# Kernel optimization log

Measured on AMD Instinct MI355X. Metric: run time of the kernel, lower is better.

The kernel has to match this reference:

```python
import jax, jax.numpy as jnp
import numpy as np
import math

NUM_HEADS = 16
ROPE_BASE = 10000.0


def _rope_cos_sin(seq_len, head_dim, dtype):
    # Qwen2-style rotary embeddings. The torch source builds cos/sin of width
    # head_dim by concatenating freqs with itself, so the first and second
    # halves are identical; the half-width table below is the equivalent math.
    half = head_dim // 2
    inv_freq = 1.0 / (ROPE_BASE ** (jnp.arange(0, head_dim, 2, dtype=jnp.float32) / head_dim))
    t = jnp.arange(seq_len, dtype=jnp.float32)
    freqs = jnp.einsum('i,j->ij', t, inv_freq)  # [S, half]
    cos = jnp.cos(freqs).astype(dtype)[None, None]  # [1,1,S,half]
    sin = jnp.sin(freqs).astype(dtype)[None, None]
    return cos, sin


def _apply_rope(x, cos, sin):
    # x: [B, H, S, D]; split-half rotation (Qwen2 rotate-half convention)
    half = x.shape[-1] // 2
    x1, x2 = x[..., :half], x[..., half:]
    return jnp.concatenate([x1 * cos - x2 * sin, x2 * cos + x1 * sin], axis=-1)


def setup_inputs() -> dict:
    key = jax.random.key(0)
    ks = jax.random.split(key, 5)
    B, S, H = 2, 2048, 2048
    scale = 1.0 / math.sqrt(H)
    return {
        'hidden_states': jax.random.normal(ks[0], (B, S, H), dtype=jnp.float32),
        'Wq': jax.random.normal(ks[1], (H, H), dtype=jnp.float32) * scale,
        'Wk': jax.random.normal(ks[2], (H, H), dtype=jnp.float32) * scale,
        'Wv': jax.random.normal(ks[3], (H, H), dtype=jnp.float32) * scale,
        'Wo': jax.random.normal(ks[4], (H, H), dtype=jnp.float32) * scale,
    }


def reference(hidden_states, Wq, Wk, Wv, Wo):
    B, S, H = hidden_states.shape
    nh = NUM_HEADS
    hd = H // nh

    def proj(W):
        # nn.Linear: x @ W.T ; then [B,S,H] -> [B,nh,S,hd]
        y = jnp.einsum('bsh,oh->bso', hidden_states, W)
        return y.reshape(B, S, nh, hd).transpose(0, 2, 1, 3)

    q, k, v = proj(Wq), proj(Wk), proj(Wv)

    cos, sin = _rope_cos_sin(S, hd, hidden_states.dtype)
    q = _apply_rope(q, cos, sin)
    k = _apply_rope(k, cos, sin)

    scores = jnp.einsum('bhqd,bhkd->bhqk', q, k) / math.sqrt(hd)
    causal = jnp.triu(jnp.full((S, S), -jnp.inf, dtype=scores.dtype), k=1)
    scores = scores + causal[None, None]
    probs = jax.nn.softmax(scores, axis=-1)

    ctx = jnp.einsum('bhqk,bhkd->bhqd', probs, v)  # [B,nh,S,hd]
    ctx = ctx.transpose(0, 2, 1, 3).reshape(B, S, H)
    out = jnp.einsum('bsh,oh->bso', ctx, Wo)
    return out
```

## Files before the change

kernel.cpp:

```cpp
#include <hip/hip_runtime.h>

#define S_LEN 2048
#define HID   2048
#define NHEAD 16
#define HD    128
#define BSZ   2
#define BS_TOT (BSZ * S_LEN)
#define QKS   4096

typedef __bf16 bf16x8 __attribute__((ext_vector_type(8)));
typedef unsigned short u16x8 __attribute__((ext_vector_type(8)));
typedef unsigned short u16x4 __attribute__((ext_vector_type(4)));
typedef float f32x4 __attribute__((ext_vector_type(4)));

static __device__ __forceinline__ bf16x8 as_bf(u16x8 v) { return __builtin_bit_cast(bf16x8, v); }

static __device__ __forceinline__ unsigned short f2bf(float f) {
  __bf16 h = (__bf16)f;
  return __builtin_bit_cast(unsigned short, h);
}
static __device__ __forceinline__ float bf2f(unsigned short b) {
  unsigned int u = ((unsigned int)b) << 16;
  return __builtin_bit_cast(float, u);
}

static __device__ __forceinline__ void gload_lds16(const unsigned short* g, unsigned short* l) {
  __builtin_amdgcn_global_load_lds((const __attribute__((address_space(1))) unsigned int*)g,
                                   (__attribute__((address_space(3))) unsigned int*)l, 16, 0, 0);
}

__global__ __launch_bounds__(256) void cvt_all(const float* __restrict__ hs,
                                               const float* __restrict__ Wq,
                                               const float* __restrict__ Wk,
                                               const float* __restrict__ Wv,
                                               const float* __restrict__ Wo,
                                               unsigned short* __restrict__ hsb,
                                               unsigned short* __restrict__ wall,
                                               float* __restrict__ ct, float* __restrict__ st) {
  int b = (int)blockIdx.x, tid = (int)threadIdx.x;
  if (b < 8192) {
    int i = b * 256 + tid;
    float4 v = ((const float4*)hs)[i];
    ushort4 o; o.x = f2bf(v.x); o.y = f2bf(v.y); o.z = f2bf(v.z); o.w = f2bf(v.w);
    ((ushort4*)hsb)[i] = o;
  } else if (b < 24576) {
    int t = b - 8192;
    int wsel = t >> 12;
    const float* in = (wsel == 0) ? Wq : (wsel == 1) ? Wk : (wsel == 2) ? Wv : Wo;
    int i = (t & 4095) * 256 + tid;
    float4 v = ((const float4*)in)[i];
    ushort4 o; o.x = f2bf(v.x); o.y = f2bf(v.y); o.z = f2bf(v.z); o.w = f2bf(v.w);
    ((ushort4*)(wall + (size_t)wsel * HID * HID))[i] = o;
  } else {
    int id = (b - 24576) * 256 + tid;
    int tt = id >> 6, d = id & 63;
    float inv = powf(10000.0f, -(float)d * (1.0f / 64.0f));
    float f = (float)tt * inv;
    float sv, cv;
    sincosf(f, &sv, &cv);
    ct[id] = cv; st[id] = sv;
  }
}

__global__ __launch_bounds__(256) void rope_apply(unsigned short* __restrict__ qk,
                                                  const float* __restrict__ ct,
                                                  const float* __restrict__ st) {
  int id = blockIdx.x * 256 + threadIdx.x;
  int d = id & 63;
  int h = (id >> 6) & (NHEAD - 1);
  int m = id >> 10;
  int s = m & (S_LEN - 1);
  float c = ct[s * 64 + d], sn = st[s * 64 + d];
  size_t base = (size_t)m * QKS + h * HD + d;
  float q1 = bf2f(qk[base]), q2 = bf2f(qk[base + 64]);
  qk[base]      = f2bf(q1 * c - q2 * sn);
  qk[base + 64] = f2bf(q2 * c + q1 * sn);
  float k1 = bf2f(qk[base + 2048]), k2 = bf2f(qk[base + 2048 + 64]);
  qk[base + 2048]      = f2bf(k1 * c - k2 * sn);
  qk[base + 2048 + 64] = f2bf(k2 * c + k1 * sn);
}

template <typename OutT>
__global__ __launch_bounds__(256) void gemm_bt(const unsigned short* __restrict__ A,
                                               const unsigned short* __restrict__ Bw,
                                               OutT* __restrict__ C, int M, int N, int K) {
  __shared__ __align__(16) unsigned short As[4][128 * 32];
  __shared__ __align__(16) unsigned short Bs[4][128 * 32];
  int x = (int)blockIdx.x;
  int chunk = (int)gridDim.x >> 3;
  int x2 = (x & 7) * chunk + (x >> 3);
  const int nbn = N >> 7;
  int bm = x2 / nbn, bn = x2 % nbn;
  int tid = (int)threadIdx.x;
  int l = tid & 63, lr = l & 15, lg = l >> 4;
  int w = tid >> 6, wm = w >> 1, wn = w & 1;

  int w32 = 32 * w;
  int srow = w32 + (l >> 2);
  int ssw = ((l >> 2) ^ (l >> 4)) & 3;
  const unsigned short* gA = A + (size_t)(bm * 128 + srow) * K + (((l & 3) ^ ssw) << 3);
  const unsigned short* gB = Bw + (size_t)(bn * 128 + srow) * K + (((l & 3) ^ ssw) << 3);

  int rsw = (lr ^ (lr >> 2)) & 3;
  int aoff[4], boff[4];
#pragma unroll
  for (int i = 0; i < 4; ++i) {
    aoff[i] = (wm * 64 + i * 16 + lr) * 32 + ((lg ^ rsw) << 3);
    boff[i] = (wn * 64 + i * 16 + lr) * 32 + ((lg ^ rsw) << 3);
  }

  f32x4 zero = {0.f, 0.f, 0.f, 0.f};
  f32x4 acc[4][4];
#pragma unroll
  for (int mi = 0; mi < 4; ++mi)
#pragma unroll
    for (int ni = 0; ni < 4; ++ni) acc[mi][ni] = zero;

  int nk = K >> 5;

#define STAGE(buf, kt)                                                        \
  do {                                                                        \
    const unsigned short* pa_ = gA + (size_t)(kt) * 32;                       \
    const unsigned short* pb_ = gB + (size_t)(kt) * 32;                       \
    gload_lds16(pa_, &As[buf][w32 * 32]);                                     \
    gload_lds16(pa_ + (size_t)16 * K, &As[buf][(w32 + 16) * 32]);             \
    gload_lds16(pb_, &Bs[buf][w32 * 32]);                                     \
    gload_lds16(pb_ + (size_t)16 * K, &Bs[buf][(w32 + 16) * 32]);             \
  } while (0)

#define COMPUTE(buf)                                                          \
  do {                                                                        \
    u16x8 af[4], bfr[4];                                                      \
    _Pragma("unroll") for (int i = 0; i < 4; ++i) {                           \
      af[i] = *(const u16x8*)&As[buf][aoff[i]];                               \
      bfr[i] = *(const u16x8*)&Bs[buf][boff[i]];                              \
    }                                                                         \
    _Pragma("unroll") for (int mi = 0; mi < 4; ++mi)                          \
        _Pragma("unroll") for (int ni = 0; ni < 4; ++ni)                      \
            acc[mi][ni] = __builtin_amdgcn_mfma_f32_16x16x32_bf16(            \
                as_bf(af[mi]), as_bf(bfr[ni]), acc[mi][ni], 0, 0, 0);         \
  } while (0)

  STAGE(0, 0);
  STAGE(1, 1);
  STAGE(2, 2);
  asm volatile("s_waitcnt vmcnt(8)" ::: "memory");
  __builtin_amdgcn_s_barrier();
#pragma unroll 4
  for (int kt = 0; kt < nk; ++kt) {
    COMPUTE(kt & 3);
    asm volatile("s_waitcnt vmcnt(4) lgkmcnt(0)" ::: "memory");
    __builtin_amdgcn_s_barrier();
    STAGE((kt + 3) & 3, (kt + 3) & (nk - 1));
  }
#undef STAGE
#undef COMPUTE

#pragma unroll
  for (int mi = 0; mi < 4; ++mi) {
#pragma unroll
    for (int ni = 0; ni < 4; ++ni) {
      int col = bn * 128 + wn * 64 + ni * 16 + lr;
#pragma unroll
      for (int j = 0; j < 4; ++j) {
        int rowm = bm * 128 + wm * 64 + mi * 16 + 4 * lg + j;
        float v = acc[mi][ni][j];
        if constexpr (sizeof(OutT) == 2) C[(size_t)rowm * N + col] = f2bf(v);
        else                             C[(size_t)rowm * N + col] = v;
      }
    }
  }
  (void)M;
}

__global__ __launch_bounds__(256, 2) void attn_fwd(const unsigned short* __restrict__ qk,
                                                   const unsigned short* __restrict__ vt,
                                                   unsigned short* __restrict__ ctx) {
  __shared__ __align__(16) unsigned short Ks[2][64 * 128];
  __shared__ __align__(16) unsigned short Vs[2][128 * 64];
  __shared__ __align__(16) unsigned short Ps[4 * 32 * 64];

  int x = (int)blockIdx.x;
  int bh, qt;
  if (x < 256) { bh = x & 31;         qt = 15 - (x >> 5); }
  else         { bh = (x - 256) & 31; qt = (x - 256) >> 5; }
  int b = bh >> 4, h = bh & 15;
  int q0 = qt * 128;
  int nt = 2 * qt + 2;

  int tid = (int)threadIdx.x;
  int w = tid >> 6, l = tid & 63, lr = l & 15, lg = l >> 4;
  const float CEXP = 0.12751744f;
  const float THRRAW = 90.509668f;
  const int bS = b * S_LEN, h128 = h * HD;
  const int qw = q0 + w * 32;
  const unsigned short* qg = qk;
  const unsigned short* kg = qk + 2048;

  u16x8 qfr[2][4];
#pragma unroll
  for (int qf = 0; qf < 2; ++qf) {
    const unsigned short* qb = qg + (size_t)(bS + qw + qf * 16 + lr) * QKS + h128;
#pragma unroll
    for (int kk = 0; kk < 4; ++kk) qfr[qf][kk] = *(const u16x8*)(qb + kk * 32 + lg * 8);
  }

  const unsigned short* kbg[4];
  const unsigned short* vbg[4];
#pragma unroll
  for (int i = 0; i < 4; ++i) {
    int rr = 16 * w + 4 * i + (l >> 4);
    int colK = ((l & 15) ^ (rr & 15)) * 8;
    kbg[i] = kg + (size_t)(bS + rr) * QKS + h128 + colK;
    int vd = 32 * w + 8 * i + (l >> 3);
    int colV = ((l & 7) ^ (vd & 7)) * 8;
    vbg[i] = vt + (size_t)(h128 + vd) * BS_TOT + bS + colV;
  }

#define ASTAGE(buf, t)                                                        \
  do {                                                                        \
    size_t koff_ = (size_t)(t) * 64 * QKS;                                    \
    int voff_ = (t) * 64;                                                     \
    _Pragma("unroll") for (int i_ = 0; i_ < 4; ++i_) {                        \
      gload_lds16(kbg[i_] + koff_, &Ks[buf][(16 * w + 4 * i_) * 128]);        \
      gload_lds16(vbg[i_] + voff_, &Vs[buf][(32 * w + 8 * i_) * 64]);         \
    }                                                                         \
  } while (0)

  f32x4 zero = {0.f, 0.f, 0.f, 0.f};
  f32x4 oacc[2][8];
#pragma unroll
  for (int qf = 0; qf < 2; ++qf)
#pragma unroll
    for (int nj = 0; nj < 8; ++nj) oacc[qf][nj] = zero;
  float mrow[2] = {-1e30f, -1e30f}, lsum[2] = {0.f, 0.f};

  int cur = 0;
  ASTAGE(0, 0);
  __syncthreads();

  for (int t = 0; t < nt; ++t) {
    int k0 = t * 64;
    if (t + 1 < nt) ASTAGE(cur ^ 1, t + 1);

    if (k0 <= qw + 31) {
      const unsigned short* KsB = &Ks[cur][0];
      const unsigned short* VsB = &Vs[cur][0];
      f32x4 sac[2][4];
#pragma unroll
      for (int qf = 0; qf < 2; ++qf)
#pragma unroll
        for (int ni = 0; ni < 4; ++ni) sac[qf][ni] = zero;
      __builtin_amdgcn_s_setprio(1);
#pragma unroll
      for (int kk = 0; kk < 4; ++kk) {
#pragma unroll
        for (int ni = 0; ni < 4; ++ni) {
          u16x8 kf = *(const u16x8*)&KsB[(ni * 16 + lr) * 128 + (((kk * 4 + lg) ^ lr) * 8)];
          sac[0][ni] = __builtin_amdgcn_mfma_f32_16x16x32_bf16(as_bf(kf), as_bf(qfr[0][kk]), sac[0][ni], 0, 0, 0);
          sac[1][ni] = __builtin_amdgcn_mfma_f32_16x16x32_bf16(as_bf(kf), as_bf(qfr[1][kk]), sac[1][ni], 0, 0, 0);
        }
      }
      __builtin_amdgcn_s_setprio(0);
      bool needmask = (k0 + 63 > qw);

#pragma unroll
      for (int qf = 0; qf < 2; ++qf) {
        float s[4][4];
#pragma unroll
        for (int ni = 0; ni < 4; ++ni)
#pragma unroll
          for (int j = 0; j < 4; ++j) s[ni][j] = sac[qf][ni][j];
        if (needmask) {
          int qgl = qw + qf * 16 + lr;
#pragma unroll
          for (int ni = 0; ni < 4; ++ni)
#pragma unroll
            for (int j = 0; j < 4; ++j)
              if (k0 + ni * 16 + 4 * lg + j > qgl) s[ni][j] = -1e30f;
        }
        float mx = s[0][0];
#pragma unroll
        for (int ni = 0; ni < 4; ++ni)
#pragma unroll
          for (int j = 0; j < 4; ++j) mx = fmaxf(mx, s[ni][j]);
        mx = fmaxf(mx, __shfl_xor(mx, 16));
        mx = fmaxf(mx, __shfl_xor(mx, 32));
        if (!__all(mx - mrow[qf] <= THRRAW)) {
          float mn = fmaxf(mrow[qf], mx);
          float al = exp2f((mrow[qf] - mn) * CEXP);
          mrow[qf] = mn;
          lsum[qf] *= al;
          float a0 = __shfl(al, 4 * lg + 0, 16);
          float a1 = __shfl(al, 4 * lg + 1, 16);
          float a2 = __shfl(al, 4 * lg + 2, 16);
          float a3 = __shfl(al, 4 * lg + 3, 16);
#pragma unroll
          for (int nj = 0; nj < 8; ++nj) {
            oacc[qf][nj][0] *= a0; oacc[qf][nj][1] *= a1;
            oacc[qf][nj][2] *= a2; oacc[qf][nj][3] *= a3;
          }
        }
        float m = mrow[qf];
        float rs = 0.f;
#pragma unroll
        for (int ni = 0; ni < 4; ++ni)
#pragma unroll
          for (int j = 0; j < 4; ++j) {
            float p = exp2f((s[ni][j] - m) * CEXP);
            s[ni][j] = p; rs += p;
          }
        lsum[qf] += rs;
        unsigned short* pw = &Ps[w * 2048];
#pragma unroll
        for (int ni = 0; ni < 4; ++ni) {
          u16x4 pv = {f2bf(s[ni][0]), f2bf(s[ni][1]), f2bf(s[ni][2]), f2bf(s[ni][3])};
          *(u16x4*)&pw[(qf * 16 + lr) * 64 + (((2 * ni + (lg >> 1)) ^ (lr & 7)) * 8) + (lg & 1) * 4] = pv;
        }
      }

      const unsigned short* pw = &Ps[w * 2048];
      __builtin_amdgcn_s_setprio(1);
#pragma unroll
      for (int kk2 = 0; kk2 < 2; ++kk2) {
        u16x8 pa0 = *(const u16x8*)&pw[(0 * 16 + lr) * 64 + (((kk2 * 4 + lg) ^ (lr & 7)) * 8)];
        u16x8 pa1 = *(const u16x8*)&pw[(1 * 16 + lr) * 64 + (((kk2 * 4 + lg) ^ (lr & 7)) * 8)];
#pragma unroll
        for (int nj = 0; nj < 8; ++nj) {
          u16x8 vf = *(const u16x8*)&VsB[(nj * 16 + lr) * 64 + (((kk2 * 4 + lg) ^ (lr & 7)) * 8)];
          oacc[0][nj] = __builtin_amdgcn_mfma_f32_16x16x32_bf16(as_bf(pa0), as_bf(vf), oacc[0][nj], 0, 0, 0);
          oacc[1][nj] = __builtin_amdgcn_mfma_f32_16x16x32_bf16(as_bf(pa1), as_bf(vf), oacc[1][nj], 0, 0, 0);
        }
      }
      __builtin_amdgcn_s_setprio(0);
    }

    __syncthreads();
    cur ^= 1;
  }
#undef ASTAGE

#pragma unroll
  for (int qf = 0; qf < 2; ++qf) {
    float ls = lsum[qf];
    ls += __shfl_xor(ls, 16);
    ls += __shfl_xor(ls, 32);
    float rl = 1.0f / ls;
    float r0 = __shfl(rl, 4 * lg + 0, 16);
    float r1 = __shfl(rl, 4 * lg + 1, 16);
    float r2 = __shfl(rl, 4 * lg + 2, 16);
    float r3 = __shfl(rl, 4 * lg + 3, 16);
    size_t obase = (size_t)(bS + qw + qf * 16 + 4 * lg) * HID + h128;
#pragma unroll
    for (int nj = 0; nj < 8; ++nj) {
      ctx[obase + 0 * HID + nj * 16 + lr] = f2bf(oacc[qf][nj][0] * r0);
      ctx[obase + 1 * HID + nj * 16 + lr] = f2bf(oacc[qf][nj][1] * r1);
      ctx[obase + 2 * HID + nj * 16 + lr] = f2bf(oacc[qf][nj][2] * r2);
      ctx[obase + 3 * HID + nj * 16 + lr] = f2bf(oacc[qf][nj][3] * r3);
    }
  }
}

extern "C" void kernel_launch(void* const* d_in, const int* in_sizes, int n_in,
                              void* d_out, int out_size, void* d_ws, size_t ws_size,
                              hipStream_t stream) {
  const float* hs = (const float*)d_in[0];
  const float* Wq = (const float*)d_in[1];
  const float* Wk = (const float*)d_in[2];
  const float* Wv = (const float*)d_in[3];
  const float* Wo = (const float*)d_in[4];

  char* ws = (char*)d_ws;
  unsigned short* hsb  = (unsigned short*)(ws);
  unsigned short* wall = (unsigned short*)(ws + 16777216);
  unsigned short* qkb  = (unsigned short*)(ws + 50331648);
  unsigned short* vtb  = (unsigned short*)(ws + 83886080);
  float* ctab = (float*)(ws + 100663296);
  float* stab = (float*)(ws + 101187584);
  unsigned short* ctxb = hsb;

  cvt_all<<<25088, 256, 0, stream>>>(hs, Wq, Wk, Wv, Wo, hsb, wall, ctab, stab);

  gemm_bt<unsigned short><<<1024, 256, 0, stream>>>(hsb, wall, qkb, BS_TOT, 2 * HID, HID);
  gemm_bt<unsigned short><<<512, 256, 0, stream>>>(wall + 2 * (size_t)HID * HID, hsb, vtb, HID, BS_TOT, HID);

  rope_apply<<<16384, 256, 0, stream>>>(qkb, ctab, stab);

  attn_fwd<<<512, 256, 0, stream>>>(qkb, vtb, ctxb);

  gemm_bt<float><<<512, 256, 0, stream>>>(ctxb, wall + 3 * (size_t)HID * HID, (float*)d_out, BS_TOT, HID, HID);

  (void)in_sizes; (void)n_in; (void)out_size; (void)ws_size;
}
```

Baseline: 296.3 us.

## Widen GEMM tile to 128x256 with triple buffering and vectorize RoPE

The GEMM tile grows from 128x128 to 128x256. Each warp now owns a full 128-row by 64-column slice, using 8x4 MFMA accumulators and a 3-stage LDS pipeline, with a manually unrolled loop and launch bounds set for 2 blocks per SM. This raises arithmetic intensity per LDS load but halves the block counts (256/512 blocks), so GPU fill and register pressure are at risk. Separately, the RoPE kernel now processes 4 elements per thread with vector loads and stores.

```diff
diff --git a/kernel.cpp b/kernel.cpp
--- a/kernel.cpp
+++ b/kernel.cpp
@@ -66,53 +66,63 @@
                                                   const float* __restrict__ ct,
                                                   const float* __restrict__ st) {
   int id = blockIdx.x * 256 + threadIdx.x;
-  int d = id & 63;
-  int h = (id >> 6) & (NHEAD - 1);
-  int m = id >> 10;
+  int d4 = (id & 15) * 4;
+  int h = (id >> 4) & (NHEAD - 1);
+  int m = id >> 8;
   int s = m & (S_LEN - 1);
-  float c = ct[s * 64 + d], sn = st[s * 64 + d];
-  size_t base = (size_t)m * QKS + h * HD + d;
-  float q1 = bf2f(qk[base]), q2 = bf2f(qk[base + 64]);
-  qk[base]      = f2bf(q1 * c - q2 * sn);
-  qk[base + 64] = f2bf(q2 * c + q1 * sn);
-  float k1 = bf2f(qk[base + 2048]), k2 = bf2f(qk[base + 2048 + 64]);
-  qk[base + 2048]      = f2bf(k1 * c - k2 * sn);
-  qk[base + 2048 + 64] = f2bf(k2 * c + k1 * sn);
+  float4 c  = *(const float4*)(ct + s * 64 + d4);
+  float4 sn = *(const float4*)(st + s * 64 + d4);
+  size_t base = (size_t)m * QKS + h * HD + d4;
+  u16x4 q1 = *(u16x4*)(qk + base), q2 = *(u16x4*)(qk + base + 64);
+  u16x4 k1 = *(u16x4*)(qk + base + 2048), k2 = *(u16x4*)(qk + base + 2048 + 64);
+  u16x4 o1, o2, p1, p2;
+  float cc[4] = {c.x, c.y, c.z, c.w}, ss[4] = {sn.x, sn.y, sn.z, sn.w};
+#pragma unroll
+  for (int j = 0; j < 4; ++j) {
+    float a = bf2f(q1[j]), bq = bf2f(q2[j]);
+    o1[j] = f2bf(a * cc[j] - bq * ss[j]);
+    o2[j] = f2bf(bq * cc[j] + a * ss[j]);
+    float ak = bf2f(k1[j]), bk = bf2f(k2[j]);
+    p1[j] = f2bf(ak * cc[j] - bk * ss[j]);
+    p2[j] = f2bf(bk * cc[j] + ak * ss[j]);
+  }
+  *(u16x4*)(qk + base) = o1;
+  *(u16x4*)(qk + base + 64) = o2;
+  *(u16x4*)(qk + base + 2048) = p1;
+  *(u16x4*)(qk + base + 2048 + 64) = p2;
 }
 
 template <typename OutT>
-__global__ __launch_bounds__(256) void gemm_bt(const unsigned short* __restrict__ A,
-                                               const unsigned short* __restrict__ Bw,
-                                               OutT* __restrict__ C, int M, int N, int K) {
-  __shared__ __align__(16) unsigned short As[4][128 * 32];
-  __shared__ __align__(16) unsigned short Bs[4][128 * 32];
+__global__ __launch_bounds__(256, 2) void gemm_bt(const unsigned short* __restrict__ A,
+                                                  const unsigned short* __restrict__ Bw,
+                                                  OutT* __restrict__ C, int M, int N, int K) {
+  __shared__ __align__(16) unsigned short As[3][128 * 32];
+  __shared__ __align__(16) unsigned short Bs[3][256 * 32];
   int x = (int)blockIdx.x;
   int chunk = (int)gridDim.x >> 3;
   int x2 = (x & 7) * chunk + (x >> 3);
-  const int nbn = N >> 7;
+  const int nbn = N >> 8;
   int bm = x2 / nbn, bn = x2 % nbn;
   int tid = (int)threadIdx.x;
   int l = tid & 63, lr = l & 15, lg = l >> 4;
-  int w = tid >> 6, wm = w >> 1, wn = w & 1;
-
-  int w32 = 32 * w;
-  int srow = w32 + (l >> 2);
+  int w = tid >> 6;
+  int w32 = 32 * w, w64 = 64 * w;
+
   int ssw = ((l >> 2) ^ (l >> 4)) & 3;
-  const unsigned short* gA = A + (size_t)(bm * 128 + srow) * K + (((l & 3) ^ ssw) << 3);
-  const unsigned short* gB = Bw + (size_t)(bn * 128 + srow) * K + (((l & 3) ^ ssw) << 3);
+  const unsigned short* gA = A + (size_t)(bm * 128 + w32 + (l >> 2)) * K + (((l & 3) ^ ssw) << 3);
+  const unsigned short* gB = Bw + (size_t)(bn * 256 + w64 + (l >> 2)) * K + (((l & 3) ^ ssw) << 3);
 
   int rsw = (lr ^ (lr >> 2)) & 3;
-  int aoff[4], boff[4];
-#pragma unroll
-  for (int i = 0; i < 4; ++i) {
-    aoff[i] = (wm * 64 + i * 16 + lr) * 32 + ((lg ^ rsw) << 3);
-    boff[i] = (wn * 64 + i * 16 + lr) * 32 + ((lg ^ rsw) << 3);
-  }
+  int aoff[8], boff[4];
+#pragma unroll
+  for (int i = 0; i < 8; ++i) aoff[i] = (i * 16 + lr) * 32 + ((lg ^ rsw) << 3);
+#pragma unroll
+  for (int i = 0; i < 4; ++i) boff[i] = (w64 + i * 16 + lr) * 32 + ((lg ^ rsw) << 3);
 
   f32x4 zero = {0.f, 0.f, 0.f, 0.f};
-  f32x4 acc[4][4];
-#pragma unroll
-  for (int mi = 0; mi < 4; ++mi)
+  f32x4 acc[8][4];
+#pragma unroll
+  for (int mi = 0; mi < 8; ++mi)
 #pragma unroll
     for (int ni = 0; ni < 4; ++ni) acc[mi][ni] = zero;
 
@@ -124,46 +134,56 @@
     const unsigned short* pb_ = gB + (size_t)(kt) * 32;                       \
     gload_lds16(pa_, &As[buf][w32 * 32]);                                     \
     gload_lds16(pa_ + (size_t)16 * K, &As[buf][(w32 + 16) * 32]);             \
-    gload_lds16(pb_, &Bs[buf][w32 * 32]);                                     \
-    gload_lds16(pb_ + (size_t)16 * K, &Bs[buf][(w32 + 16) * 32]);             \
+    gload_lds16(pb_, &Bs[buf][w64 * 32]);                                     \
+    gload_lds16(pb_ + (size_t)16 * K, &Bs[buf][(w64 + 16) * 32]);             \
+    gload_lds16(pb_ + (size_t)32 * K, &Bs[buf][(w64 + 32) * 32]);             \
+    gload_lds16(pb_ + (size_t)48 * K, &Bs[buf][(w64 + 48) * 32]);             \
   } while (0)
 
 #define COMPUTE(buf)                                                          \
   do {                                                                        \
-    u16x8 af[4], bfr[4];                                                      \
-    _Pragma("unroll") for (int i = 0; i < 4; ++i) {                           \
-      af[i] = *(const u16x8*)&As[buf][aoff[i]];                               \
-      bfr[i] = *(const u16x8*)&Bs[buf][boff[i]];                              \
-    }                                                                         \
-    _Pragma("unroll") for (int mi = 0; mi < 4; ++mi)                          \
+    u16x8 af[8], bfr[4];                                                      \
+    _Pragma("unroll") for (int i = 0; i < 8; ++i)                             \
+        af[i] = *(const u16x8*)&As[buf][aoff[i]];                             \
+    _Pragma("unroll") for (int i = 0; i < 4; ++i)                             \
+        bfr[i] = *(const u16x8*)&Bs[buf][boff[i]];                            \
+    _Pragma("unroll") for (int mi = 0; mi < 8; ++mi)                          \
         _Pragma("unroll") for (int ni = 0; ni < 4; ++ni)                      \
             acc[mi][ni] = __builtin_amdgcn_mfma_f32_16x16x32_bf16(            \
                 as_bf(af[mi]), as_bf(bfr[ni]), acc[mi][ni], 0, 0, 0);         \
   } while (0)
 
+#define BODY(b)                                                               \
+  do {                                                                        \
+    COMPUTE(b);                                                               \
+    asm volatile("s_waitcnt vmcnt(6) lgkmcnt(0)" ::: "memory");               \
+    __builtin_amdgcn_s_barrier();                                             \
+    STAGE(b, (kt + 3) & (nk - 1));                                            \
+    ++kt;                                                                     \
+  } while (0)
+
   STAGE(0, 0);
   STAGE(1, 1);
   STAGE(2, 2);
-  asm volatile("s_waitcnt vmcnt(8)" ::: "memory");
+  asm volatile("s_waitcnt vmcnt(12)" ::: "memory");
   __builtin_amdgcn_s_barrier();
-#pragma unroll 4
-  for (int kt = 0; kt < nk; ++kt) {
-    COMPUTE(kt & 3);
-    asm volatile("s_waitcnt vmcnt(4) lgkmcnt(0)" ::: "memory");
-    __builtin_amdgcn_s_barrier();
-    STAGE((kt + 3) & 3, (kt + 3) & (nk - 1));
-  }
+
+  int kt = 0;
+  while (kt + 3 <= nk) { BODY(0); BODY(1); BODY(2); }
+  if (kt < nk) BODY(0);
+  if (kt < nk) BODY(1);
+#undef BODY
 #undef STAGE
 #undef COMPUTE
 
 #pragma unroll
-  for (int mi = 0; mi < 4; ++mi) {
+  for (int mi = 0; mi < 8; ++mi) {
 #pragma unroll
     for (int ni = 0; ni < 4; ++ni) {
-      int col = bn * 128 + wn * 64 + ni * 16 + lr;
+      int col = bn * 256 + w64 + ni * 16 + lr;
 #pragma unroll
       for (int j = 0; j < 4; ++j) {
-        int rowm = bm * 128 + wm * 64 + mi * 16 + 4 * lg + j;
+        int rowm = bm * 128 + mi * 16 + 4 * lg + j;
         float v = acc[mi][ni][j];
         if constexpr (sizeof(OutT) == 2) C[(size_t)rowm * N + col] = f2bf(v);
         else                             C[(size_t)rowm * N + col] = v;
@@ -381,14 +401,14 @@
 
   cvt_all<<<25088, 256, 0, stream>>>(hs, Wq, Wk, Wv, Wo, hsb, wall, ctab, stab);
 
-  gemm_bt<unsigned short><<<1024, 256, 0, stream>>>(hsb, wall, qkb, BS_TOT, 2 * HID, HID);
-  gemm_bt<unsigned short><<<512, 256, 0, stream>>>(wall + 2 * (size_t)HID * HID, hsb, vtb, HID, BS_TOT, HID);
-
-  rope_apply<<<16384, 256, 0, stream>>>(qkb, ctab, stab);
+  gemm_bt<unsigned short><<<512, 256, 0, stream>>>(hsb, wall, qkb, BS_TOT, 2 * HID, HID);
+  gemm_bt<unsigned short><<<256, 256, 0, stream>>>(wall + 2 * (size_t)HID * HID, hsb, vtb, HID, BS_TOT, HID);
+
+  rope_apply<<<4096, 256, 0, stream>>>(qkb, ctab, stab);
 
   attn_fwd<<<512, 256, 0, stream>>>(qkb, vtb, ctxb);
 
-  gemm_bt<float><<<512, 256, 0, stream>>>(ctxb, wall + 3 * (size_t)HID * HID, (float*)d_out, BS_TOT, HID, HID);
+  gemm_bt<float><<<256, 256, 0, stream>>>(ctxb, wall + 3 * (size_t)HID * HID, (float*)d_out, BS_TOT, HID, HID);
 
   (void)in_sizes; (void)n_in; (void)out_size; (void)ws_size;
 }
```

New measurement: 316.5 us. 1.07x slower.

## Add 256x256-tile GEMM for QK projection and vectorize RoPE kernel

Applied to the files above, without the earlier changes.

Adds a new 512-thread GEMM kernel with 256x256 output tiles, BK=64 double-buffered LDS staging with XOR swizzle and setprio around MFMA bursts. It is used for the fused Q/K projection to raise arithmetic intensity per block. The RoPE kernel also now processes four elements per thread with vector loads and stores, cutting its launch to a quarter of the threads. The large tile produces only 256 blocks on a 256-CU device, which gives a single wave with no tail but leaves little latency hiding per CU.

```diff
diff --git a/kernel.cpp b/kernel.cpp
--- a/kernel.cpp
+++ b/kernel.cpp
@@ -66,22 +66,131 @@
                                                   const float* __restrict__ ct,
                                                   const float* __restrict__ st) {
   int id = blockIdx.x * 256 + threadIdx.x;
-  int d = id & 63;
-  int h = (id >> 6) & (NHEAD - 1);
-  int m = id >> 10;
+  int d4 = (id & 15) * 4;
+  int h = (id >> 4) & (NHEAD - 1);
+  int m = id >> 8;
   int s = m & (S_LEN - 1);
-  float c = ct[s * 64 + d], sn = st[s * 64 + d];
-  size_t base = (size_t)m * QKS + h * HD + d;
-  float q1 = bf2f(qk[base]), q2 = bf2f(qk[base + 64]);
-  qk[base]      = f2bf(q1 * c - q2 * sn);
-  qk[base + 64] = f2bf(q2 * c + q1 * sn);
-  float k1 = bf2f(qk[base + 2048]), k2 = bf2f(qk[base + 2048 + 64]);
-  qk[base + 2048]      = f2bf(k1 * c - k2 * sn);
-  qk[base + 2048 + 64] = f2bf(k2 * c + k1 * sn);
+  float4 c  = *(const float4*)(ct + s * 64 + d4);
+  float4 sn = *(const float4*)(st + s * 64 + d4);
+  size_t base = (size_t)m * QKS + h * HD + d4;
+  u16x4 q1 = *(u16x4*)(qk + base), q2 = *(u16x4*)(qk + base + 64);
+  u16x4 k1 = *(u16x4*)(qk + base + 2048), k2 = *(u16x4*)(qk + base + 2048 + 64);
+  u16x4 o1, o2, p1, p2;
+  float cc[4] = {c.x, c.y, c.z, c.w}, ss[4] = {sn.x, sn.y, sn.z, sn.w};
+#pragma unroll
+  for (int j = 0; j < 4; ++j) {
+    float a = bf2f(q1[j]), bq = bf2f(q2[j]);
+    o1[j] = f2bf(a * cc[j] - bq * ss[j]);
+    o2[j] = f2bf(bq * cc[j] + a * ss[j]);
+    float ak = bf2f(k1[j]), bk = bf2f(k2[j]);
+    p1[j] = f2bf(ak * cc[j] - bk * ss[j]);
+    p2[j] = f2bf(bk * cc[j] + ak * ss[j]);
+  }
+  *(u16x4*)(qk + base) = o1;
+  *(u16x4*)(qk + base + 64) = o2;
+  *(u16x4*)(qk + base + 2048) = p1;
+  *(u16x4*)(qk + base + 2048 + 64) = p2;
 }
 
 template <typename OutT>
-__global__ __launch_bounds__(256) void gemm_bt(const unsigned short* __restrict__ A,
+__global__ __launch_bounds__(512, 1) void gemm256(const unsigned short* __restrict__ A,
+                                                  const unsigned short* __restrict__ Bw,
+                                                  OutT* __restrict__ C, int M, int N, int K) {
+  __shared__ __align__(16) unsigned short As[2][256 * 64];
+  __shared__ __align__(16) unsigned short Bs[2][256 * 64];
+  int x = (int)blockIdx.x;
+  int chunk = (int)gridDim.x >> 3;
+  int x2 = (x & 7) * chunk + (x >> 3);
+  const int nbn = N >> 8;
+  int bm = x2 / nbn, bn = x2 % nbn;
+  int tid = (int)threadIdx.x;
+  int l = tid & 63, lr = l & 15, lg = l >> 4;
+  int w = tid >> 6;
+  int wm = w >> 2, wn = w & 3;
+
+  int srow = 32 * w + (l >> 3);
+  int sslot = (l & 7) ^ ((l >> 3) & 7);
+  const unsigned short* gA = A + (size_t)(bm * 256 + srow) * K + sslot * 8;
+  const unsigned short* gB = Bw + (size_t)(bn * 256 + srow) * K + sslot * 8;
+
+  int rs7 = lr & 7;
+
+  f32x4 zero = {0.f, 0.f, 0.f, 0.f};
+  f32x4 acc[8][4];
+#pragma unroll
+  for (int mi = 0; mi < 8; ++mi)
+#pragma unroll
+    for (int ni = 0; ni < 4; ++ni) acc[mi][ni] = zero;
+
+  int nk = K >> 6;
+
+#define STAGE256(buf, kt)                                                       \
+  do {                                                                          \
+    size_t ko_ = (size_t)(kt) * 64;                                             \
+    _Pragma("unroll") for (int i_ = 0; i_ < 4; ++i_) {                          \
+      gload_lds16(gA + (size_t)(8 * i_) * K + ko_, &As[buf][(32 * w + 8 * i_) * 64]); \
+      gload_lds16(gB + (size_t)(8 * i_) * K + ko_, &Bs[buf][(32 * w + 8 * i_) * 64]); \
+    }                                                                           \
+  } while (0)
+
+  STAGE256(0, 0);
+  __syncthreads();
+
+  for (int kt = 0; kt < nk; ++kt) {
+    if (kt + 1 < nk) STAGE256((kt + 1) & 1, kt + 1);
+    const unsigned short* Ab = &As[kt & 1][0];
+    const unsigned short* Bb = &Bs[kt & 1][0];
+
+    u16x8 bfr[4][2];
+#pragma unroll
+    for (int ni = 0; ni < 4; ++ni)
+#pragma unroll
+      for (int ks = 0; ks < 2; ++ks)
+        bfr[ni][ks] = *(const u16x8*)&Bb[(wn * 64 + ni * 16 + lr) * 64 + (((ks * 4 + lg) ^ rs7) * 8)];
+
+#pragma unroll
+    for (int mq = 0; mq < 4; ++mq) {
+      u16x8 af[2][2];
+#pragma unroll
+      for (int m2 = 0; m2 < 2; ++m2)
+#pragma unroll
+        for (int ks = 0; ks < 2; ++ks)
+          af[m2][ks] = *(const u16x8*)&Ab[(wm * 128 + (2 * mq + m2) * 16 + lr) * 64 + (((ks * 4 + lg) ^ rs7) * 8)];
+      __builtin_amdgcn_s_setprio(1);
+#pragma unroll
+      for (int m2 = 0; m2 < 2; ++m2)
+#pragma unroll
+        for (int ni = 0; ni < 4; ++ni)
+#pragma unroll
+          for (int ks = 0; ks < 2; ++ks)
+            acc[2 * mq + m2][ni] = __builtin_amdgcn_mfma_f32_16x16x32_bf16(
+                as_bf(af[m2][ks]), as_bf(bfr[ni][ks]), acc[2 * mq + m2][ni], 0, 0, 0);
+      __builtin_amdgcn_s_setprio(0);
+      __builtin_amdgcn_s_barrier();
+    }
+    __syncthreads();
+  }
+#undef STAGE256
+
+#pragma unroll
+  for (int mi = 0; mi < 8; ++mi) {
+#pragma unroll
+    for (int ni = 0; ni < 4; ++ni) {
+      int col = bn * 256 + wn * 64 + ni * 16 + lr;
+#pragma unroll
+      for (int j = 0; j < 4; ++j) {
+        int rowm = bm * 256 + wm * 128 + mi * 16 + 4 * lg + j;
+        float v = acc[mi][ni][j];
+        if constexpr (sizeof(OutT) == 2) C[(size_t)rowm * N + col] = f2bf(v);
+        else                             C[(size_t)rowm * N + col] = v;
+      }
+    }
+  }
+  (void)M;
+}
+
+template <typename OutT>
+__global__ __launch_bounds__(256) void gemm128(const unsigned short* __restrict__ A,
                                                const unsigned short* __restrict__ Bw,
                                                OutT* __restrict__ C, int M, int N, int K) {
   __shared__ __align__(16) unsigned short As[4][128 * 32];
@@ -381,14 +490,14 @@
 
   cvt_all<<<25088, 256, 0, stream>>>(hs, Wq, Wk, Wv, Wo, hsb, wall, ctab, stab);
 
-  gemm_bt<unsigned short><<<1024, 256, 0, stream>>>(hsb, wall, qkb, BS_TOT, 2 * HID, HID);
-  gemm_bt<unsigned short><<<512, 256, 0, stream>>>(wall + 2 * (size_t)HID * HID, hsb, vtb, HID, BS_TOT, HID);
-
-  rope_apply<<<16384, 256, 0, stream>>>(qkb, ctab, stab);
+  gemm256<unsigned short><<<256, 512, 0, stream>>>(hsb, wall, qkb, BS_TOT, 2 * HID, HID);
+  gemm128<unsigned short><<<512, 256, 0, stream>>>(wall + 2 * (size_t)HID * HID, hsb, vtb, HID, BS_TOT, HID);
+
+  rope_apply<<<4096, 256, 0, stream>>>(qkb, ctab, stab);
 
   attn_fwd<<<512, 256, 0, stream>>>(qkb, vtb, ctxb);
 
-  gemm_bt<float><<<512, 256, 0, stream>>>(ctxb, wall + 3 * (size_t)HID * HID, (float*)d_out, BS_TOT, HID, HID);
+  gemm128<float><<<512, 256, 0, stream>>>(ctxb, wall + 3 * (size_t)HID * HID, (float*)d_out, BS_TOT, HID, HID);
 
   (void)in_sizes; (void)n_in; (void)out_size; (void)ws_size;
 }
```

Measured after the change: 281.6 us. 5.0% less time.
